# Performance work log

Hardware: AMD Instinct MI355X
Metric: run time of the kernel (lower is better)

## Reference

```python
import jax, jax.numpy as jnp
import numpy as np

SEQ, BATCH = 256, 8
N_NODES = SEQ * BATCH
VOCAB, D_MODEL, H, D_K, D_FF, N_LAYERS, MAX_POS = 259, 256, 8, 32, 1024, 2, 128


def setup_inputs() -> dict:
    key = jax.random.key(0)
    ks = jax.random.split(key, 16)
    # structured causal edge list per sequence (dst attends to src <= dst, incl. self)
    tri_dst, tri_src = np.tril_indices(SEQ)
    offs = (np.arange(BATCH) * SEQ)[:, None]
    edge_src = jnp.asarray((tri_src[None, :] + offs).ravel(), dtype=jnp.int64)
    edge_dst = jnp.asarray((tri_dst[None, :] + offs).ravel(), dtype=jnp.int64)
    positions = jnp.tile(jnp.arange(SEQ, dtype=jnp.int64), BATCH)
    tokens = jax.random.randint(ks[0], (N_NODES,), 0, VOCAB, dtype=jnp.int64)
    s = 0.02
    p = lambda k, shp: jax.random.normal(k, shp, dtype=jnp.float32) * s
    return {
        "tokens": tokens, "positions": positions,
        "edge_src": edge_src, "edge_dst": edge_dst,
        "coord_emb": p(ks[1], (3, D_MODEL)),
        "pos_emb": p(ks[2], (MAX_POS, D_MODEL)),
        "value_emb": p(ks[3], (VOCAB, D_MODEL)),
        "ln1_scale": jnp.ones((N_LAYERS, D_MODEL)), "ln1_bias": jnp.zeros((N_LAYERS, D_MODEL)),
        "Wqkv": p(ks[4], (N_LAYERS, D_MODEL, 3 * D_MODEL)),
        "Wo": p(ks[5], (N_LAYERS, D_MODEL, D_MODEL)),
        "ln2_scale": jnp.ones((N_LAYERS, D_MODEL)), "ln2_bias": jnp.zeros((N_LAYERS, D_MODEL)),
        "W1": p(ks[6], (N_LAYERS, D_MODEL, D_FF)), "b1": jnp.zeros((N_LAYERS, D_FF)),
        "W2": p(ks[7], (N_LAYERS, D_FF, D_MODEL)), "b2": jnp.zeros((N_LAYERS, D_MODEL)),
        "lnf_scale": jnp.ones((D_MODEL,)), "lnf_bias": jnp.zeros((D_MODEL,)),
        "Wg": p(ks[8], (D_MODEL, VOCAB)), "bg": jnp.zeros((VOCAB,)),
    }


def _ln(x, scale, bias, eps=1e-5):
    mu = jnp.mean(x, axis=-1, keepdims=True)
    var = jnp.var(x, axis=-1, keepdims=True)
    return (x - mu) * jax.lax.rsqrt(var + eps) * scale + bias


def _graph_attention(x, src, dst, Wqkv, Wo, ln_s, ln_b):
    n = x.shape[0]
    xn = _ln(x, ln_s, ln_b)
    qkv = (xn @ Wqkv).reshape(n, 3, H, D_K)
    q, k, v = qkv[:, 0], qkv[:, 1], qkv[:, 2]  # [n, H, D_K] each
    # u_dot_v('k','q','score') per edge, scaled
    score = jnp.einsum("ehd,ehd->eh", k[src], q[dst]) / jnp.sqrt(jnp.float32(D_K))
    # edge_softmax over incoming edges of each dst node
    smax = jax.ops.segment_max(score, dst, num_segments=n)      # [n, H]
    ex = jnp.exp(score - smax[dst])                              # [E, H]
    denom = jax.ops.segment_sum(ex, dst, num_segments=n)        # [n, H]
    alpha = ex / denom[dst]
    # u_mul_e('v','softmax_score') + sum reduce -> z on dst nodes
    z = jax.ops.segment_sum(alpha[:, :, None] * v[src], dst, num_segments=n)  # [n, H, D_K]
    return x + z.reshape(n, D_MODEL) @ Wo


def reference(tokens, positions, edge_src, edge_dst, coord_emb, pos_emb, value_emb,
              ln1_scale, ln1_bias, Wqkv, Wo, ln2_scale, ln2_bias, W1, b1, W2, b2,
              lnf_scale, lnf_bias, Wg, bg):
    x = coord_emb[positions % 3] + pos_emb[positions // 3] + value_emb[tokens]
    for i in range(Wqkv.shape[0]):
        x = _graph_attention(x, edge_src, edge_dst, Wqkv[i], Wo[i], ln1_scale[i], ln1_bias[i])
        h = _ln(x, ln2_scale[i], ln2_bias[i])
        x = x + jax.nn.relu(h @ W1[i] + b1[i]) @ W2[i] + b2[i]
    out = _ln(x, lnf_scale, lnf_bias) @ Wg + bg
    return jax.nn.log_softmax(out, axis=-1)
```

## Files before the change

### kernel.cpp

```cpp
#include <hip/hip_runtime.h>
#include <hip/hip_bf16.h>

typedef __hip_bfloat16 bf16;
typedef unsigned short ushort_t;
typedef unsigned int uint_t;
typedef __attribute__((ext_vector_type(8))) short short8;
typedef __attribute__((ext_vector_type(4))) float floatx4;

#define D_MODEL 256
#define SEQ     256
#define BATCH   8
#define NN      2048
#define NHEAD   8
#define DK      32
#define DFF     1024
#define VOCAB   259
#define NLAYER  2

#define WQKVT_OFF 0
#define WOT_OFF   393216
#define W1T_OFF   524288
#define W2T_OFF   1048576
#define WGT_OFF   1572864
#define WT_TOTAL  1639168
#define LNP_TOTAL 2560
#define BP_TOTAL  2819

__device__ __forceinline__ ushort_t f2bs(float f) {
    bf16 h = __float2bfloat16(f);
    ushort_t u; __builtin_memcpy(&u, &h, 2); return u;
}
template<bool BF>
__device__ __forceinline__ float ldw(const void* p, int i) {
    if (BF) return __bfloat162float(((const bf16*)p)[i]);
    return ((const float*)p)[i];
}
template<bool BF>
__device__ __forceinline__ ushort_t ldb(const void* p, size_t i) {
    if (BF) return ((const ushort_t*)p)[i];
    return f2bs(((const float*)p)[i]);
}
template<bool I64>
__device__ __forceinline__ int ldi(const void* p, int i) {
    if (I64) return (int)(((const long long*)p)[i]);
    return ((const int*)p)[i];
}
__device__ __forceinline__ float wred_sum(float v) {
    #pragma unroll
    for (int m = 32; m > 0; m >>= 1) v += __shfl_xor(v, m, 64);
    return v;
}
__device__ __forceinline__ float wred_max(float v) {
    #pragma unroll
    for (int m = 32; m > 0; m >>= 1) v = fmaxf(v, __shfl_xor(v, m, 64));
    return v;
}
__device__ __forceinline__ bool detBF(const void* ln1s) {
    return *(const uint_t*)ln1s == 0x3F803F80u;
}
__device__ __forceinline__ bool detI64(const void* pos) {
    const int* p32 = (const int*)pos;
    return p32[1] == 0 && p32[2] == 1;
}

template<bool BF>
__device__ void ttile(const void* src, size_t srcOff, int K, int N, int tk, int tn,
                      ushort_t* dst, ushort_t (*tile)[68]) {
    int t = threadIdx.x;
    #pragma unroll
    for (int pass = 0; pass < 16; ++pass) {
        int e = pass * 256 + t;
        int kl = e >> 6, nl = e & 63;
        int n = tn * 64 + nl;
        tile[kl][nl] = (n < N) ? ldb<BF>(src, srcOff + (size_t)(tk*64 + kl) * N + n)
                               : (ushort_t)0;
    }
    __syncthreads();
    #pragma unroll
    for (int pass = 0; pass < 16; ++pass) {
        int e = pass * 256 + t;
        int nl = e >> 6, kl = e & 63;
        int n = tn * 64 + nl;
        if (n < N) dst[(size_t)n * K + tk*64 + kl] = tile[kl][nl];
    }
}

template<bool BF, bool I64>
__device__ void embedln16(const void* tok, const void* pos,
        const void* ce, const void* pe, const void* ve,
        const void* ln1s, const void* ln1b, int rowBase,
        float* x, ushort_t* xn) {
    int lane = threadIdx.x & 63, wave = threadIdx.x >> 6;
    #pragma unroll
    for (int i = 0; i < 4; ++i) {
        int n = rowBase + wave * 4 + i;
        int p  = ldi<I64>(pos, n);
        int tk = ldi<I64>(tok, n);
        int c0 = lane * 4;
        float v[4];
        #pragma unroll
        for (int j = 0; j < 4; ++j)
            v[j] = ldw<BF>(ce, (p % 3) * 256 + c0 + j)
                 + ldw<BF>(pe, (p / 3) * 256 + c0 + j)
                 + ldw<BF>(ve, tk * 256 + c0 + j);
        float s  = wred_sum(v[0] + v[1] + v[2] + v[3]);
        float s2 = wred_sum(v[0]*v[0] + v[1]*v[1] + v[2]*v[2] + v[3]*v[3]);
        float mu = s * (1.f/256.f);
        float var = s2 * (1.f/256.f) - mu * mu;
        float rstd = rsqrtf(var + 1e-5f);
        *reinterpret_cast<float4*>(&x[(size_t)n*256 + c0]) =
            make_float4(v[0], v[1], v[2], v[3]);
        ushort4 o;
        o.x = f2bs((v[0]-mu)*rstd*ldw<BF>(ln1s, c0+0) + ldw<BF>(ln1b, c0+0));
        o.y = f2bs((v[1]-mu)*rstd*ldw<BF>(ln1s, c0+1) + ldw<BF>(ln1b, c0+1));
        o.z = f2bs((v[2]-mu)*rstd*ldw<BF>(ln1s, c0+2) + ldw<BF>(ln1b, c0+2));
        o.w = f2bs((v[3]-mu)*rstd*ldw<BF>(ln1s, c0+3) + ldw<BF>(ln1b, c0+3));
        *reinterpret_cast<ushort4*>(&xn[(size_t)n*256 + c0]) = o;
    }
}

template<bool BF, bool I64>
__device__ void prep_body(const void* tok, const void* pos,
        const void* ce, const void* pe, const void* ve,
        const void* Wqkv, const void* Wo, const void* W1, const void* W2, const void* Wg,
        const void* ln1s, const void* ln1b, const void* ln2s, const void* ln2b,
        const void* lnfs, const void* lnfb,
        const void* b1, const void* b2, const void* bg,
        ushort_t* WT, float* lnP, float* bP, float* x, ushort_t* xn,
        ushort_t (*tile)[68]) {
    int blk = blockIdx.x;
    if (blk < 404) {
        const void* src; int K, N, tk, tn; size_t dstOff, srcOff;
        if (blk < 96)       { int L = blk/48, lo = blk%48; src=Wqkv; K=256; N=768;
                              srcOff=(size_t)L*196608; dstOff=WQKVT_OFF+(size_t)L*196608;
                              tk=lo/12; tn=lo%12; }
        else if (blk < 128) { int b2=blk-96, L=b2/16, lo=b2%16; src=Wo; K=256; N=256;
                              srcOff=(size_t)L*65536; dstOff=WOT_OFF+(size_t)L*65536;
                              tk=lo/4; tn=lo%4; }
        else if (blk < 256) { int b2=blk-128, L=b2/64, lo=b2%64; src=W1; K=256; N=1024;
                              srcOff=(size_t)L*262144; dstOff=W1T_OFF+(size_t)L*262144;
                              tk=lo/16; tn=lo%16; }
        else if (blk < 384) { int b2=blk-256, L=b2/64, lo=b2%64; src=W2; K=1024; N=256;
                              srcOff=(size_t)L*262144; dstOff=W2T_OFF+(size_t)L*262144;
                              tk=lo/4; tn=lo%4; }
        else                { int lo=blk-384; src=Wg; K=256; N=259;
                              srcOff=0; dstOff=WGT_OFF; tk=lo/5; tn=lo%5; }
        ttile<BF>(src, srcOff, K, N, tk, tn, WT + dstOff, tile);
    } else if (blk < 426) {
        int gid = (blk - 404) * 256 + threadIdx.x;
        if (gid < LNP_TOTAL) {
            float v;
            if      (gid < 512)  v = ldw<BF>(ln1s, gid);
            else if (gid < 1024) v = ldw<BF>(ln1b, gid - 512);
            else if (gid < 1536) v = ldw<BF>(ln2s, gid - 1024);
            else if (gid < 2048) v = ldw<BF>(ln2b, gid - 1536);
            else if (gid < 2304) v = ldw<BF>(lnfs, gid - 2048);
            else                 v = ldw<BF>(lnfb, gid - 2304);
            lnP[gid] = v;
        } else if (gid < LNP_TOTAL + BP_TOTAL) {
            int g = gid - LNP_TOTAL;
            float v;
            if      (g < 2048) v = ldw<BF>(b1, g);
            else if (g < 2560) v = ldw<BF>(b2, g - 2048);
            else               v = ldw<BF>(bg, g - 2560);
            bP[g] = v;
        }
    } else {
        embedln16<BF, I64>(tok, pos, ce, pe, ve, ln1s, ln1b, (blk - 426) * 16, x, xn);
    }
}

__global__ void __launch_bounds__(256) prep_k(const void* tok, const void* pos,
        const void* ce, const void* pe, const void* ve,
        const void* Wqkv, const void* Wo, const void* W1, const void* W2, const void* Wg,
        const void* ln1s, const void* ln1b, const void* ln2s, const void* ln2b,
        const void* lnfs, const void* lnfb,
        const void* b1, const void* b2, const void* bg,
        ushort_t* WT, float* lnP, float* bP, float* x, ushort_t* xn) {
    __shared__ ushort_t tile[64][68];
    bool BF = detBF(ln1s), I64 = detI64(pos);
    if (BF) { if (I64) prep_body<true,true >(tok,pos,ce,pe,ve,Wqkv,Wo,W1,W2,Wg,ln1s,ln1b,ln2s,ln2b,lnfs,lnfb,b1,b2,bg,WT,lnP,bP,x,xn,tile);
              else     prep_body<true,false>(tok,pos,ce,pe,ve,Wqkv,Wo,W1,W2,Wg,ln1s,ln1b,ln2s,ln2b,lnfs,lnfb,b1,b2,bg,WT,lnP,bP,x,xn,tile); }
    else    { if (I64) prep_body<false,true >(tok,pos,ce,pe,ve,Wqkv,Wo,W1,W2,Wg,ln1s,ln1b,ln2s,ln2b,lnfs,lnfb,b1,b2,bg,WT,lnP,bP,x,xn,tile);
              else     prep_body<false,false>(tok,pos,ce,pe,ve,Wqkv,Wo,W1,W2,Wg,ln1s,ln1b,ln2s,ln2b,lnfs,lnfb,b1,b2,bg,WT,lnP,bP,x,xn,tile); }
}

union AttnSH {
    struct {
        ushort_t Ks[SEQ][40];
        ushort_t Qs[64][40];
    } a;
    ushort_t Ps[64][264];
};
__global__ void __launch_bounds__(256) attn_k(const ushort_t* __restrict__ qkvB,
                                              ushort_t* __restrict__ zB) {
    __shared__ AttnSH u;
    __shared__ ushort_t Vt[32][264];
    int t = threadIdx.x;
    int lane = t & 63, wave = t >> 6;
    int quad = lane >> 4, l16 = lane & 15;
    int tile = blockIdx.x & 3, bh = blockIdx.x >> 2;
    int b = bh >> 3, h = bh & 7;
    int base = b * SEQ;
    int dstBase = tile * 64;
    int tileEnd = (tile + 1) * 64;

    int nV = tileEnd * 4;
    for (int i = t; i < nV; i += 256) {
        int src = i >> 2, g = i & 3;
        const ushort_t* rp = qkvB + (size_t)(base + src) * 768 + h * 32 + g * 8;
        uint4 kv = *reinterpret_cast<const uint4*>(rp + 256);
        *reinterpret_cast<uint4*>(&u.a.Ks[src][g * 8]) = kv;
        uint4 vv = *reinterpret_cast<const uint4*>(rp + 512);
        const ushort_t* vs = (const ushort_t*)&vv;
        #pragma unroll
        for (int j = 0; j < 8; ++j) Vt[g * 8 + j][src] = vs[j];
    }
    {
        int r = t >> 2, g = t & 3;
        uint4 qv = *reinterpret_cast<const uint4*>(
            qkvB + (size_t)(base + dstBase + r) * 768 + h * 32 + g * 8);
        *reinterpret_cast<uint4*>(&u.a.Qs[r][g * 8]) = qv;
    }
    __syncthreads();

    const float scale = 0.17677669529663687f;
    int stLim = tile * 4 + wave;
    int stCnt = stLim + 1;
    short8 qf = *reinterpret_cast<const short8*>(&u.a.Qs[wave * 16 + l16][quad * 8]);
    floatx4 accs[16];
    #pragma unroll
    for (int st = 0; st < 16; ++st) {
        if (st <= stLim) {
            short8 kf = *reinterpret_cast<const short8*>(&u.a.Ks[st * 16 + l16][quad * 8]);
            accs[st] = __builtin_amdgcn_mfma_f32_16x16x32_bf16(qf, kf, (floatx4){0.f,0.f,0.f,0.f}, 0, 0, 0);
        }
    }
    float mrow[4] = {-3e38f, -3e38f, -3e38f, -3e38f};
    #pragma unroll
    for (int st = 0; st < 16; ++st) {
        if (st <= stLim) {
            int srcg = st * 16 + l16;
            #pragma unroll
            for (int r = 0; r < 4; ++r) {
                int dstg = dstBase + wave * 16 + quad * 4 + r;
                float sv = (srcg <= dstg) ? accs[st][r] * scale : -3e38f;
                accs[st][r] = sv;
                mrow[r] = fmaxf(mrow[r], sv);
            }
        }
    }
    #pragma unroll
    for (int mk = 1; mk < 16; mk <<= 1)
        #pragma unroll
        for (int r = 0; r < 4; ++r) mrow[r] = fmaxf(mrow[r], __shfl_xor(mrow[r], mk, 64));
    float lrow[4] = {0.f, 0.f, 0.f, 0.f};
    #pragma unroll
    for (int st = 0; st < 16; ++st) {
        if (st <= stLim) {
            #pragma unroll
            for (int r = 0; r < 4; ++r) {
                float p = __expf(accs[st][r] - mrow[r]);
                accs[st][r] = p;
                lrow[r] += p;
            }
        }
    }
    #pragma unroll
    for (int mk = 1; mk < 16; mk <<= 1)
        #pragma unroll
        for (int r = 0; r < 4; ++r) lrow[r] += __shfl_xor(lrow[r], mk, 64);
    __syncthreads();

    #pragma unroll
    for (int st = 0; st < 16; ++st) {
        if (st <= stLim) {
            #pragma unroll
            for (int r = 0; r < 4; ++r)
                u.Ps[wave * 16 + quad * 4 + r][st * 16 + l16] = f2bs(accs[st][r]);
        }
    }
    if (stCnt & 1) {
        #pragma unroll
        for (int r = 0; r < 4; ++r)
            u.Ps[wave * 16 + quad * 4 + r][stCnt * 16 + l16] = 0;
    }
    __syncthreads();

    int ktCnt = (stCnt + 1) >> 1;
    floatx4 acco[2];
    acco[0] = (floatx4){0.f,0.f,0.f,0.f};
    acco[1] = (floatx4){0.f,0.f,0.f,0.f};
    #pragma unroll
    for (int kt = 0; kt < 8; ++kt) {
        if (kt < ktCnt) {
            short8 pf = *reinterpret_cast<const short8*>(&u.Ps[wave * 16 + l16][kt * 32 + quad * 8]);
            #pragma unroll
            for (int dn = 0; dn < 2; ++dn) {
                short8 vf = *reinterpret_cast<const short8*>(&Vt[dn * 16 + l16][kt * 32 + quad * 8]);
                acco[dn] = __builtin_amdgcn_mfma_f32_16x16x32_bf16(pf, vf, acco[dn], 0, 0, 0);
            }
        }
    }
    #pragma unroll
    for (int dn = 0; dn < 2; ++dn)
        #pragma unroll
        for (int r = 0; r < 4; ++r)
            zB[(size_t)(base + dstBase + wave * 16 + quad * 4 + r) * 256
               + h * 32 + dn * 16 + l16] = f2bs(acco[dn][r] / lrow[r]);
}

__global__ void __launch_bounds__(256) gemm_k(const ushort_t* __restrict__ A, int K,
        const ushort_t* __restrict__ BT, const float* __restrict__ bias,
        ushort_t* __restrict__ C, int ldc, int relu) {
    int t = threadIdx.x;
    int lane = t & 63, wave = t >> 6;
    int quad = lane >> 4, l16 = lane & 15;
    int wm = (wave >> 1) * 32, wn = (wave & 1) * 32;
    int rowBase = blockIdx.x * 64, colBase = blockIdx.y * 64;
    floatx4 acc[2][2];
    #pragma unroll
    for (int a = 0; a < 2; ++a)
        #pragma unroll
        for (int b = 0; b < 2; ++b) acc[a][b] = (floatx4){0.f,0.f,0.f,0.f};
    const ushort_t* a0 = A + (size_t)(rowBase + wm + l16) * K + quad * 8;
    const ushort_t* a1 = a0 + (size_t)16 * K;
    const ushort_t* b0 = BT + (size_t)(colBase + wn + l16) * K + quad * 8;
    const ushort_t* b1 = b0 + (size_t)16 * K;
    #pragma unroll 8
    for (int k0 = 0; k0 < K; k0 += 32) {
        short8 af0 = *reinterpret_cast<const short8*>(a0 + k0);
        short8 af1 = *reinterpret_cast<const short8*>(a1 + k0);
        short8 bf0 = *reinterpret_cast<const short8*>(b0 + k0);
        short8 bf1 = *reinterpret_cast<const short8*>(b1 + k0);
        acc[0][0] = __builtin_amdgcn_mfma_f32_16x16x32_bf16(af0, bf0, acc[0][0], 0,0,0);
        acc[0][1] = __builtin_amdgcn_mfma_f32_16x16x32_bf16(af0, bf1, acc[0][1], 0,0,0);
        acc[1][0] = __builtin_amdgcn_mfma_f32_16x16x32_bf16(af1, bf0, acc[1][0], 0,0,0);
        acc[1][1] = __builtin_amdgcn_mfma_f32_16x16x32_bf16(af1, bf1, acc[1][1], 0,0,0);
    }
    #pragma unroll
    for (int nt = 0; nt < 2; ++nt) {
        int col = colBase + wn + nt*16 + l16;
        float bb = bias ? bias[col] : 0.f;
        #pragma unroll
        for (int mt = 0; mt < 2; ++mt)
            #pragma unroll
            for (int r = 0; r < 4; ++r) {
                int row = rowBase + wm + mt*16 + quad*4 + r;
                float v = acc[mt][nt][r] + bb;
                if (relu) v = fmaxf(v, 0.f);
                C[(size_t)row * ldc + col] = f2bs(v);
            }
    }
}

__global__ void __launch_bounds__(256) woff1_k(
        const ushort_t* __restrict__ zB, const ushort_t* __restrict__ WoT,
        const float* __restrict__ xIn, float* __restrict__ xOut,
        const float* __restrict__ ls2, const float* __restrict__ lb2,
        const ushort_t* __restrict__ W1T, const float* __restrict__ b1P,
        ushort_t* __restrict__ hmidG) {
    __shared__ float    xrow[32][256];
    __shared__ ushort_t xnA[32][264];
    int t = threadIdx.x, lane = t & 63, wave = t >> 6;
    int quad = lane >> 4, l16 = lane & 15;
    int rowBase = blockIdx.x * 32, cg = blockIdx.y;

    {
        floatx4 acc[2][4];
        #pragma unroll
        for (int mt = 0; mt < 2; ++mt)
            #pragma unroll
            for (int nt = 0; nt < 4; ++nt) acc[mt][nt] = (floatx4){0.f,0.f,0.f,0.f};
        const ushort_t* a0 = zB + (size_t)(rowBase + l16) * 256 + quad * 8;
        const ushort_t* a1 = a0 + (size_t)16 * 256;
        #pragma unroll
        for (int k0 = 0; k0 < 256; k0 += 32) {
            short8 af0 = *reinterpret_cast<const short8*>(a0 + k0);
            short8 af1 = *reinterpret_cast<const short8*>(a1 + k0);
            #pragma unroll
            for (int nt = 0; nt < 4; ++nt) {
                short8 bv = *reinterpret_cast<const short8*>(
                    WoT + (size_t)(wave*64 + nt*16 + l16) * 256 + k0 + quad * 8);
                acc[0][nt] = __builtin_amdgcn_mfma_f32_16x16x32_bf16(af0, bv, acc[0][nt], 0,0,0);
                acc[1][nt] = __builtin_amdgcn_mfma_f32_16x16x32_bf16(af1, bv, acc[1][nt], 0,0,0);
            }
        }
        #pragma unroll
        for (int nt = 0; nt < 4; ++nt) {
            int col = wave*64 + nt*16 + l16;
            #pragma unroll
            for (int mt = 0; mt < 2; ++mt)
                #pragma unroll
                for (int r = 0; r < 4; ++r) {
                    int row = mt*16 + quad*4 + r;
                    float v = acc[mt][nt][r] + xIn[(size_t)(rowBase + row) * 256 + col];
                    xOut[(size_t)(rowBase + row) * 256 + col] = v;
                    xrow[row][col] = v;
                }
        }
    }
    __syncthreads();
    #pragma unroll
    for (int i = 0; i < 8; ++i) {
        int row = wave*8 + i, c0 = lane * 4;
        float4 vv = *reinterpret_cast<const float4*>(&xrow[row][c0]);
        float s  = wred_sum(vv.x + vv.y + vv.z + vv.w);
        float s2 = wred_sum(vv.x*vv.x + vv.y*vv.y + vv.z*vv.z + vv.w*vv.w);
        float mu = s * (1.f/256.f);
        float var = s2 * (1.f/256.f) - mu*mu;
        float rstd = rsqrtf(var + 1e-5f);
        ushort4 o;
        o.x = f2bs((vv.x-mu)*rstd*ls2[c0+0] + lb2[c0+0]);
        o.y = f2bs((vv.y-mu)*rstd*ls2[c0+1] + lb2[c0+1]);
        o.z = f2bs((vv.z-mu)*rstd*ls2[c0+2] + lb2[c0+2]);
        o.w = f2bs((vv.w-mu)*rstd*ls2[c0+3] + lb2[c0+3]);
        *reinterpret_cast<ushort4*>(&xnA[row][c0]) = o;
    }
    __syncthreads();
    {
        floatx4 acc[2][4];
        #pragma unroll
        for (int mt = 0; mt < 2; ++mt)
            #pragma unroll
            for (int nt = 0; nt < 4; ++nt) acc[mt][nt] = (floatx4){0.f,0.f,0.f,0.f};
        const ushort_t* a0 = &xnA[l16][quad * 8];
        const ushort_t* a1 = &xnA[16 + l16][quad * 8];
        #pragma unroll
        for (int k0 = 0; k0 < 256; k0 += 32) {
            short8 af0 = *reinterpret_cast<const short8*>(a0 + k0);
            short8 af1 = *reinterpret_cast<const short8*>(a1 + k0);
            #pragma unroll
            for (int nt = 0; nt < 4; ++nt) {
                short8 bv = *reinterpret_cast<const short8*>(
                    W1T + (size_t)(cg*256 + wave*64 + nt*16 + l16) * 256 + k0 + quad * 8);
                acc[0][nt] = __builtin_amdgcn_mfma_f32_16x16x32_bf16(af0, bv, acc[0][nt], 0,0,0);
                acc[1][nt] = __builtin_amdgcn_mfma_f32_16x16x32_bf16(af1, bv, acc[1][nt], 0,0,0);
            }
        }
        #pragma unroll
        for (int nt = 0; nt < 4; ++nt) {
            int col = cg*256 + wave*64 + nt*16 + l16;
            float bb = b1P[col];
            #pragma unroll
            for (int mt = 0; mt < 2; ++mt)
                #pragma unroll
                for (int r = 0; r < 4; ++r) {
                    int row = mt*16 + quad*4 + r;
                    hmidG[(size_t)(rowBase + row) * 1024 + col] =
                        f2bs(fmaxf(acc[mt][nt][r] + bb, 0.f));
                }
        }
    }
}

__global__ void __launch_bounds__(256) w2_k(
        const ushort_t* __restrict__ hmidG, const ushort_t* __restrict__ W2T,
        const float* __restrict__ b2P,
        const float* __restrict__ xPre, float* __restrict__ yOut) {
    int t = threadIdx.x, lane = t & 63, wave = t >> 6;
    int quad = lane >> 4, l16 = lane & 15;
    int rowBase = blockIdx.x * 32, colBase = blockIdx.y * 64;
    int wm = (wave >> 1) * 16, wn = (wave & 1) * 32;
    floatx4 acc[2];
    acc[0] = (floatx4){0.f,0.f,0.f,0.f};
    acc[1] = (floatx4){0.f,0.f,0.f,0.f};
    const ushort_t* a0 = hmidG + (size_t)(rowBase + wm + l16) * 1024 + quad * 8;
    #pragma unroll 8
    for (int k0 = 0; k0 < 1024; k0 += 32) {
        short8 af = *reinterpret_cast<const short8*>(a0 + k0);
        #pragma unroll
        for (int nt = 0; nt < 2; ++nt) {
            short8 bv = *reinterpret_cast<const short8*>(
                W2T + (size_t)(colBase + wn + nt*16 + l16) * 1024 + k0 + quad * 8);
            acc[nt] = __builtin_amdgcn_mfma_f32_16x16x32_bf16(af, bv, acc[nt], 0,0,0);
        }
    }
    #pragma unroll
    for (int nt = 0; nt < 2; ++nt) {
        int col = colBase + wn + nt*16 + l16;
        float bb = b2P[col];
        #pragma unroll
        for (int r = 0; r < 4; ++r) {
            int row = wm + quad*4 + r;
            float v = acc[nt][r] + bb + xPre[(size_t)(rowBase + row) * 256 + col];
            yOut[(size_t)(rowBase + row) * 256 + col] = v;
        }
    }
}

__global__ void __launch_bounds__(256) lnqkv_k(
        const float* __restrict__ yIn,
        const float* __restrict__ ls, const float* __restrict__ lb,
        const ushort_t* __restrict__ WqkvT, ushort_t* __restrict__ qkvB) {
    __shared__ ushort_t xnA[64][264];
    int t = threadIdx.x, lane = t & 63, wave = t >> 6;
    int quad = lane >> 4, l16 = lane & 15;
    int rowBase = blockIdx.x * 64, colBase = blockIdx.y * 64;
    #pragma unroll
    for (int i = 0; i < 16; ++i) {
        int row = wave*16 + i, c0 = lane * 4;
        float4 vv = *reinterpret_cast<const float4*>(yIn + (size_t)(rowBase + row) * 256 + c0);
        float s  = wred_sum(vv.x + vv.y + vv.z + vv.w);
        float s2 = wred_sum(vv.x*vv.x + vv.y*vv.y + vv.z*vv.z + vv.w*vv.w);
        float mu = s * (1.f/256.f);
        float var = s2 * (1.f/256.f) - mu*mu;
        float rstd = rsqrtf(var + 1e-5f);
        ushort4 o;
        o.x = f2bs((vv.x-mu)*rstd*ls[c0+0] + lb[c0+0]);
        o.y = f2bs((vv.y-mu)*rstd*ls[c0+1] + lb[c0+1]);
        o.z = f2bs((vv.z-mu)*rstd*ls[c0+2] + lb[c0+2]);
        o.w = f2bs((vv.w-mu)*rstd*ls[c0+3] + lb[c0+3]);
        *reinterpret_cast<ushort4*>(&xnA[row][c0]) = o;
    }
    __syncthreads();
    int wm = (wave >> 1) * 32, wn = (wave & 1) * 32;
    floatx4 acc[2][2];
    #pragma unroll
    for (int a = 0; a < 2; ++a)
        #pragma unroll
        for (int b = 0; b < 2; ++b) acc[a][b] = (floatx4){0.f,0.f,0.f,0.f};
    const ushort_t* a0 = &xnA[wm + l16][quad * 8];
    const ushort_t* a1 = &xnA[wm + 16 + l16][quad * 8];
    #pragma unroll
    for (int k0 = 0; k0 < 256; k0 += 32) {
        short8 af0 = *reinterpret_cast<const short8*>(a0 + k0);
        short8 af1 = *reinterpret_cast<const short8*>(a1 + k0);
        #pragma unroll
        for (int nt = 0; nt < 2; ++nt) {
            short8 bv = *reinterpret_cast<const short8*>(
                WqkvT + (size_t)(colBase + wn + nt*16 + l16) * 256 + k0 + quad * 8);
            acc[0][nt] = __builtin_amdgcn_mfma_f32_16x16x32_bf16(af0, bv, acc[0][nt], 0,0,0);
            acc[1][nt] = __builtin_amdgcn_mfma_f32_16x16x32_bf16(af1, bv, acc[1][nt], 0,0,0);
        }
    }
    #pragma unroll
    for (int nt = 0; nt < 2; ++nt) {
        int col = colBase + wn + nt*16 + l16;
        #pragma unroll
        for (int mt = 0; mt < 2; ++mt)
            #pragma unroll
            for (int r = 0; r < 4; ++r) {
                int row = wm + mt*16 + quad*4 + r;
                qkvB[(size_t)(rowBase + row) * 768 + col] = f2bs(acc[mt][nt][r]);
            }
    }
}

__global__ void __launch_bounds__(256) lnlg_k(
        const float* __restrict__ yIn,
        const float* __restrict__ lnfsP, const float* __restrict__ lnfbP,
        const ushort_t* __restrict__ WgT, const float* __restrict__ bgP,
        const void* __restrict__ ln1sRaw, void* __restrict__ outp) {
    __shared__ float    xrow[16][256];
    __shared__ ushort_t xnA[16][264];
    __shared__ float    Lg[16][273];
    int t = threadIdx.x, lane = t & 63, wave = t >> 6;
    int quad = lane >> 4, l16 = lane & 15;
    int rowBase = blockIdx.x * 16;
    #pragma unroll
    for (int i = 0; i < 4; ++i) {
        int idx = i * 256 + t;
        int row = idx >> 6, c4 = (idx & 63) * 4;
        *reinterpret_cast<float4*>(&xrow[row][c4]) =
            *reinterpret_cast<const float4*>(yIn + (size_t)(rowBase + row) * 256 + c4);
    }
    __syncthreads();
    #pragma unroll
    for (int i = 0; i < 4; ++i) {
        int row = wave*4 + i, c0 = lane * 4;
        float4 vv = *reinterpret_cast<const float4*>(&xrow[row][c0]);
        float s  = wred_sum(vv.x + vv.y + vv.z + vv.w);
        float s2 = wred_sum(vv.x*vv.x + vv.y*vv.y + vv.z*vv.z + vv.w*vv.w);
        float mu = s * (1.f/256.f);
        float var = s2 * (1.f/256.f) - mu*mu;
        float rstd = rsqrtf(var + 1e-5f);
        ushort4 o;
        o.x = f2bs((vv.x-mu)*rstd*lnfsP[c0+0] + lnfbP[c0+0]);
        o.y = f2bs((vv.y-mu)*rstd*lnfsP[c0+1] + lnfbP[c0+1]);
        o.z = f2bs((vv.z-mu)*rstd*lnfsP[c0+2] + lnfbP[c0+2]);
        o.w = f2bs((vv.w-mu)*rstd*lnfsP[c0+3] + lnfbP[c0+3]);
        *reinterpret_cast<ushort4*>(&xnA[row][c0]) = o;
    }
    __syncthreads();
    const ushort_t* a0 = &xnA[l16][quad * 8];
    int cb = wave * 64;
    {
        floatx4 acc[4];
        #pragma unroll
        for (int nt = 0; nt < 4; ++nt) acc[nt] = (floatx4){0.f,0.f,0.f,0.f};
        #pragma unroll
        for (int kc = 0; kc < 8; ++kc) {
            short8 af = *reinterpret_cast<const short8*>(a0 + kc * 32);
            #pragma unroll
            for (int nt = 0; nt < 4; ++nt) {
                short8 bv = *reinterpret_cast<const short8*>(
                    WgT + (size_t)(cb + nt*16 + l16) * 256 + kc*32 + quad*8);
                acc[nt] = __builtin_amdgcn_mfma_f32_16x16x32_bf16(af, bv, acc[nt], 0,0,0);
            }
        }
        #pragma unroll
        for (int nt = 0; nt < 4; ++nt) {
            int col = cb + nt*16 + l16;
            float bb = bgP[col];
            #pragma unroll
            for (int r = 0; r < 4; ++r)
                Lg[quad*4 + r][col] = acc[nt][r] + bb;
        }
    }
    if (wave == 0) {
        floatx4 acc = (floatx4){0.f,0.f,0.f,0.f};
        int n = 256 + l16;
        int nc = (n < VOCAB) ? n : 0;
        const ushort_t* b0 = WgT + (size_t)nc * 256 + quad * 8;
        #pragma unroll
        for (int kc = 0; kc < 8; ++kc) {
            short8 af = *reinterpret_cast<const short8*>(a0 + kc * 32);
            short8 bv = *reinterpret_cast<const short8*>(b0 + kc * 32);
            acc = __builtin_amdgcn_mfma_f32_16x16x32_bf16(af, bv, acc, 0,0,0);
        }
        #pragma unroll
        for (int r = 0; r < 4; ++r)
            Lg[quad*4 + r][256 + l16] = (n < VOCAB) ? (acc[r] + bgP[n]) : -1e30f;
    }
    __syncthreads();
    int outBF = detBF(ln1sRaw) ? 1 : 0;
    #pragma unroll
    for (int i = 0; i < 4; ++i) {
        int row = wave*4 + i;
        float v0 = Lg[row][lane],     v1 = Lg[row][lane+64];
        float v2 = Lg[row][lane+128], v3 = Lg[row][lane+192];
        float v4 = (lane < 16) ? Lg[row][256+lane] : -1e30f;
        float m = wred_max(fmaxf(fmaxf(fmaxf(v0,v1), fmaxf(v2,v3)), v4));
        float se = __expf(v0-m) + __expf(v1-m) + __expf(v2-m) + __expf(v3-m)
                 + ((lane < 16) ? __expf(v4-m) : 0.f);
        se = wred_sum(se);
        float lse = m + logf(se);
        size_t nbase = (size_t)(rowBase + row) * VOCAB;
        if (outBF) {
            ushort_t* o = (ushort_t*)outp + nbase;
            o[lane]     = f2bs(v0 - lse);
            o[lane+64]  = f2bs(v1 - lse);
            o[lane+128] = f2bs(v2 - lse);
            o[lane+192] = f2bs(v3 - lse);
            if (lane < 3) o[256+lane] = f2bs(v4 - lse);
        } else {
            float* o = (float*)outp + nbase;
            o[lane]     = v0 - lse;
            o[lane+64]  = v1 - lse;
            o[lane+128] = v2 - lse;
            o[lane+192] = v3 - lse;
            if (lane < 3) o[256+lane] = v4 - lse;
        }
    }
}

extern "C" void kernel_launch(void* const* d_in, const int* in_sizes, int n_in,
                              void* d_out, int out_size, void* d_ws, size_t ws_size,
                              hipStream_t stream) {
    const void* tok  = d_in[0];
    const void* pos  = d_in[1];
    const void* ce   = d_in[4];
    const void* pe   = d_in[5];
    const void* ve   = d_in[6];
    const void* ln1s = d_in[7];
    const void* ln1b = d_in[8];
    const void* Wqkv = d_in[9];
    const void* Wo   = d_in[10];
    const void* ln2s = d_in[11];
    const void* ln2b = d_in[12];
    const void* W1   = d_in[13];
    const void* b1   = d_in[14];
    const void* W2   = d_in[15];
    const void* b2   = d_in[16];
    const void* lnfs = d_in[17];
    const void* lnfb = d_in[18];
    const void* Wg   = d_in[19];
    const void* bg   = d_in[20];

    char* base = (char*)d_ws;
    float*    lnP   = (float*)base;
    float*    bP    = (float*)(base + 10240);
    float*    xA    = (float*)(base + 22528);
    ushort_t* xn    = (ushort_t*)(base + 2119680);
    ushort_t* zB    = (ushort_t*)(base + 3168256);
    ushort_t* hmidG = (ushort_t*)(base + 4216832);
    ushort_t* WT    = (ushort_t*)(base + 8411136);
    ushort_t* qkvB  = (ushort_t*)(base + 11689472);
    float*    xB    = (float*)(base + 14835200);
    float*    xC    = (float*)(base + 16932352);

    prep_k<<<554, 256, 0, stream>>>(tok, pos, ce, pe, ve,
        Wqkv, Wo, W1, W2, Wg, ln1s, ln1b, ln2s, ln2b, lnfs, lnfb,
        b1, b2, bg, WT, lnP, bP, xA, xn);

    gemm_k<<<dim3(32, 12), 256, 0, stream>>>(xn, 256,
        WT + WQKVT_OFF, nullptr, qkvB, 768, 0);

    attn_k<<<256, 256, 0, stream>>>(qkvB, zB);

    woff1_k<<<dim3(64, 4), 256, 0, stream>>>(zB, WT + WOT_OFF, xA, xB,
        lnP + 1024, lnP + 1536, WT + W1T_OFF, bP, hmidG);
    w2_k<<<dim3(64, 4), 256, 0, stream>>>(hmidG, WT + W2T_OFF, bP + 2048, xB, xC);

    lnqkv_k<<<dim3(32, 12), 256, 0, stream>>>(xC, lnP + 256, lnP + 768,
        WT + WQKVT_OFF + 196608, qkvB);

    attn_k<<<256, 256, 0, stream>>>(qkvB, zB);

    woff1_k<<<dim3(64, 4), 256, 0, stream>>>(zB, WT + WOT_OFF + 65536, xC, xA,
        lnP + 1024 + 256, lnP + 1536 + 256, WT + W1T_OFF + 262144, bP + 1024, hmidG);
    w2_k<<<dim3(64, 4), 256, 0, stream>>>(hmidG, WT + W2T_OFF + 262144,
        bP + 2048 + 256, xA, xB);

    lnlg_k<<<128, 256, 0, stream>>>(xB, lnP + 2048, lnP + 2304,
        WT + WGT_OFF, bP + 2560, ln1s, d_out);
}
```

Before: 212.0 us.

## Fuse FFN down-projection into Wo/W1 kernel with split-K atomic accumulation

Merges the W2 GEMM into the Wo+LN2+W1 kernel: each column-group block keeps its 256-wide slice of the hidden activation in shared memory and computes a split-K partial of W2, accumulated into the output with float atomics. The attention kernel zeroes the output buffer beforehand, and the cg==0 block adds the residual and bias. This removes one launch per layer and the global round-trip of the hidden activation. It also vectorizes the weight-transpose prep path for 64-aligned widths. The atomics add contention and make the summation order nondeterministic.

Measured after the change: 204.3 us. 1.04x faster.

```diff
diff --git a/kernel.cpp b/kernel.cpp
--- a/kernel.cpp
+++ b/kernel.cpp
@@ -65,23 +65,55 @@
 
 template<bool BF>
 __device__ void ttile(const void* src, size_t srcOff, int K, int N, int tk, int tn,
-                      ushort_t* dst, ushort_t (*tile)[68]) {
+                      ushort_t* dst, ushort_t (*tile)[72]) {
     int t = threadIdx.x;
-    #pragma unroll
-    for (int pass = 0; pass < 16; ++pass) {
-        int e = pass * 256 + t;
-        int kl = e >> 6, nl = e & 63;
-        int n = tn * 64 + nl;
-        tile[kl][nl] = (n < N) ? ldb<BF>(src, srcOff + (size_t)(tk*64 + kl) * N + n)
-                               : (ushort_t)0;
-    }
-    __syncthreads();
-    #pragma unroll
-    for (int pass = 0; pass < 16; ++pass) {
-        int e = pass * 256 + t;
-        int nl = e >> 6, kl = e & 63;
-        int n = tn * 64 + nl;
-        if (n < N) dst[(size_t)n * K + tk*64 + kl] = tile[kl][nl];
+    if ((N & 63) == 0) {
+        #pragma unroll
+        for (int pass = 0; pass < 2; ++pass) {
+            int e = pass * 256 + t;
+            int kl = e >> 3, ng = e & 7;
+            size_t sbase = srcOff + (size_t)(tk*64 + kl) * N + tn*64 + ng*8;
+            ushort_t v[8];
+            if (BF) {
+                *reinterpret_cast<uint4*>(v) =
+                    *reinterpret_cast<const uint4*>((const ushort_t*)src + sbase);
+            } else {
+                float4 a = *reinterpret_cast<const float4*>((const float*)src + sbase);
+                float4 b = *reinterpret_cast<const float4*>((const float*)src + sbase + 4);
+                v[0]=f2bs(a.x); v[1]=f2bs(a.y); v[2]=f2bs(a.z); v[3]=f2bs(a.w);
+                v[4]=f2bs(b.x); v[5]=f2bs(b.y); v[6]=f2bs(b.z); v[7]=f2bs(b.w);
+            }
+            *reinterpret_cast<uint4*>(&tile[kl][ng*8]) = *reinterpret_cast<const uint4*>(v);
+        }
+        __syncthreads();
+        #pragma unroll
+        for (int pass = 0; pass < 2; ++pass) {
+            int e = pass * 256 + t;
+            int nl = e >> 3, kg = e & 7;
+            int n = tn * 64 + nl;
+            ushort_t v[8];
+            #pragma unroll
+            for (int j = 0; j < 8; ++j) v[j] = tile[kg*8 + j][nl];
+            *reinterpret_cast<uint4*>(dst + (size_t)n * K + tk*64 + kg*8) =
+                *reinterpret_cast<const uint4*>(v);
+        }
+    } else {
+        #pragma unroll
+        for (int pass = 0; pass < 16; ++pass) {
+            int e = pass * 256 + t;
+            int kl = e >> 6, nl = e & 63;
+            int n = tn * 64 + nl;
+            tile[kl][nl] = (n < N) ? ldb<BF>(src, srcOff + (size_t)(tk*64 + kl) * N + n)
+                                   : (ushort_t)0;
+        }
+        __syncthreads();
+        #pragma unroll
+        for (int pass = 0; pass < 16; ++pass) {
+            int e = pass * 256 + t;
+            int nl = e >> 6, kl = e & 63;
+            int n = tn * 64 + nl;
+            if (n < N) dst[(size_t)n * K + tk*64 + kl] = tile[kl][nl];
+        }
     }
 }
 
@@ -127,7 +159,7 @@
         const void* lnfs, const void* lnfb,
         const void* b1, const void* b2, const void* bg,
         ushort_t* WT, float* lnP, float* bP, float* x, ushort_t* xn,
-        ushort_t (*tile)[68]) {
+        ushort_t (*tile)[72]) {
     int blk = blockIdx.x;
     if (blk < 404) {
         const void* src; int K, N, tk, tn; size_t dstOff, srcOff;
@@ -177,7 +209,7 @@
         const void* lnfs, const void* lnfb,
         const void* b1, const void* b2, const void* bg,
         ushort_t* WT, float* lnP, float* bP, float* x, ushort_t* xn) {
-    __shared__ ushort_t tile[64][68];
+    __shared__ ushort_t tile[64][72];
     bool BF = detBF(ln1s), I64 = detI64(pos);
     if (BF) { if (I64) prep_body<true,true >(tok,pos,ce,pe,ve,Wqkv,Wo,W1,W2,Wg,ln1s,ln1b,ln2s,ln2b,lnfs,lnfb,b1,b2,bg,WT,lnP,bP,x,xn,tile);
               else     prep_body<true,false>(tok,pos,ce,pe,ve,Wqkv,Wo,W1,W2,Wg,ln1s,ln1b,ln2s,ln2b,lnfs,lnfb,b1,b2,bg,WT,lnP,bP,x,xn,tile); }
@@ -193,10 +225,17 @@
     ushort_t Ps[64][264];
 };
 __global__ void __launch_bounds__(256) attn_k(const ushort_t* __restrict__ qkvB,
-                                              ushort_t* __restrict__ zB) {
+                                              ushort_t* __restrict__ zB,
+                                              float* __restrict__ yZ) {
     __shared__ AttnSH u;
     __shared__ ushort_t Vt[32][264];
     int t = threadIdx.x;
+    {
+        float4 z4 = make_float4(0.f, 0.f, 0.f, 0.f);
+        float4* yp = reinterpret_cast<float4*>(yZ + (size_t)blockIdx.x * 2048);
+        yp[t]       = z4;
+        yp[t + 256] = z4;
+    }
     int lane = t & 63, wave = t >> 6;
     int quad = lane >> 4, l16 = lane & 15;
     int tile = blockIdx.x & 3, bh = blockIdx.x >> 2;
@@ -354,17 +393,20 @@
     }
 }
 
-__global__ void __launch_bounds__(256) woff1_k(
+__global__ void __launch_bounds__(256) tail_k(
         const ushort_t* __restrict__ zB, const ushort_t* __restrict__ WoT,
-        const float* __restrict__ xIn, float* __restrict__ xOut,
+        const float* __restrict__ xIn,
         const float* __restrict__ ls2, const float* __restrict__ lb2,
         const ushort_t* __restrict__ W1T, const float* __restrict__ b1P,
-        ushort_t* __restrict__ hmidG) {
-    __shared__ float    xrow[32][256];
+        const ushort_t* __restrict__ W2T, const float* __restrict__ b2P,
+        float* __restrict__ yAcc) {
+    __shared__ float    xrowS[32][256];
     __shared__ ushort_t xnA[32][264];
+    ushort_t (*hmidS)[264] = reinterpret_cast<ushort_t (*)[264]>(&xrowS[0][0]);
     int t = threadIdx.x, lane = t & 63, wave = t >> 6;
     int quad = lane >> 4, l16 = lane & 15;
     int rowBase = blockIdx.x * 32, cg = blockIdx.y;
+    float vpre[2][4][4];
 
     {
         floatx4 acc[2][4];
@@ -395,8 +437,8 @@
                 for (int r = 0; r < 4; ++r) {
                     int row = mt*16 + quad*4 + r;
                     float v = acc[mt][nt][r] + xIn[(size_t)(rowBase + row) * 256 + col];
-                    xOut[(size_t)(rowBase + row) * 256 + col] = v;
-                    xrow[row][col] = v;
+                    vpre[mt][nt][r] = v;
+                    xrowS[row][col] = v;
                 }
         }
     }
@@ -404,7 +446,7 @@
     #pragma unroll
     for (int i = 0; i < 8; ++i) {
         int row = wave*8 + i, c0 = lane * 4;
-        float4 vv = *reinterpret_cast<const float4*>(&xrow[row][c0]);
+        float4 vv = *reinterpret_cast<const float4*>(&xrowS[row][c0]);
         float s  = wred_sum(vv.x + vv.y + vv.z + vv.w);
         float s2 = wred_sum(vv.x*vv.x + vv.y*vv.y + vv.z*vv.z + vv.w*vv.w);
         float mu = s * (1.f/256.f);
@@ -418,6 +460,7 @@
         *reinterpret_cast<ushort4*>(&xnA[row][c0]) = o;
     }
     __syncthreads();
+
     {
         floatx4 acc[2][4];
         #pragma unroll
@@ -438,53 +481,55 @@
                 acc[1][nt] = __builtin_amdgcn_mfma_f32_16x16x32_bf16(af1, bv, acc[1][nt], 0,0,0);
             }
         }
+        __syncthreads();
         #pragma unroll
         for (int nt = 0; nt < 4; ++nt) {
-            int col = cg*256 + wave*64 + nt*16 + l16;
-            float bb = b1P[col];
+            int lcol = wave*64 + nt*16 + l16;
+            float bb = b1P[cg*256 + lcol];
             #pragma unroll
             for (int mt = 0; mt < 2; ++mt)
                 #pragma unroll
                 for (int r = 0; r < 4; ++r) {
                     int row = mt*16 + quad*4 + r;
-                    hmidG[(size_t)(rowBase + row) * 1024 + col] =
-                        f2bs(fmaxf(acc[mt][nt][r] + bb, 0.f));
+                    hmidS[row][lcol] = f2bs(fmaxf(acc[mt][nt][r] + bb, 0.f));
                 }
         }
     }
-}
-
-__global__ void __launch_bounds__(256) w2_k(
-        const ushort_t* __restrict__ hmidG, const ushort_t* __restrict__ W2T,
-        const float* __restrict__ b2P,
-        const float* __restrict__ xPre, float* __restrict__ yOut) {
-    int t = threadIdx.x, lane = t & 63, wave = t >> 6;
-    int quad = lane >> 4, l16 = lane & 15;
-    int rowBase = blockIdx.x * 32, colBase = blockIdx.y * 64;
-    int wm = (wave >> 1) * 16, wn = (wave & 1) * 32;
-    floatx4 acc[2];
-    acc[0] = (floatx4){0.f,0.f,0.f,0.f};
-    acc[1] = (floatx4){0.f,0.f,0.f,0.f};
-    const ushort_t* a0 = hmidG + (size_t)(rowBase + wm + l16) * 1024 + quad * 8;
-    #pragma unroll 8
-    for (int k0 = 0; k0 < 1024; k0 += 32) {
-        short8 af = *reinterpret_cast<const short8*>(a0 + k0);
-        #pragma unroll
-        for (int nt = 0; nt < 2; ++nt) {
-            short8 bv = *reinterpret_cast<const short8*>(
-                W2T + (size_t)(colBase + wn + nt*16 + l16) * 1024 + k0 + quad * 8);
-            acc[nt] = __builtin_amdgcn_mfma_f32_16x16x32_bf16(af, bv, acc[nt], 0,0,0);
-        }
-    }
-    #pragma unroll
-    for (int nt = 0; nt < 2; ++nt) {
-        int col = colBase + wn + nt*16 + l16;
-        float bb = b2P[col];
-        #pragma unroll
-        for (int r = 0; r < 4; ++r) {
-            int row = wm + quad*4 + r;
-            float v = acc[nt][r] + bb + xPre[(size_t)(rowBase + row) * 256 + col];
-            yOut[(size_t)(rowBase + row) * 256 + col] = v;
+    __syncthreads();
+
+    {
+        floatx4 acc[2][4];
+        #pragma unroll
+        for (int mt = 0; mt < 2; ++mt)
+            #pragma unroll
+            for (int nt = 0; nt < 4; ++nt) acc[mt][nt] = (floatx4){0.f,0.f,0.f,0.f};
+        const ushort_t* a0 = &hmidS[l16][quad * 8];
+        const ushort_t* a1 = &hmidS[16 + l16][quad * 8];
+        #pragma unroll
+        for (int k0 = 0; k0 < 256; k0 += 32) {
+            short8 af0 = *reinterpret_cast<const short8*>(a0 + k0);
+            short8 af1 = *reinterpret_cast<const short8*>(a1 + k0);
+            #pragma unroll
+            for (int nt = 0; nt < 4; ++nt) {
+                short8 bv = *reinterpret_cast<const short8*>(
+                    W2T + (size_t)(wave*64 + nt*16 + l16) * 1024 + cg*256 + k0 + quad * 8);
+                acc[0][nt] = __builtin_amdgcn_mfma_f32_16x16x32_bf16(af0, bv, acc[0][nt], 0,0,0);
+                acc[1][nt] = __builtin_amdgcn_mfma_f32_16x16x32_bf16(af1, bv, acc[1][nt], 0,0,0);
+            }
+        }
+        #pragma unroll
+        for (int nt = 0; nt < 4; ++nt) {
+            int col = wave*64 + nt*16 + l16;
+            float bb = (cg == 0) ? b2P[col] : 0.f;
+            #pragma unroll
+            for (int mt = 0; mt < 2; ++mt)
+                #pragma unroll
+                for (int r = 0; r < 4; ++r) {
+                    int row = mt*16 + quad*4 + r;
+                    float add = acc[mt][nt][r];
+                    if (cg == 0) add += vpre[mt][nt][r] + bb;
+                    atomicAdd(&yAcc[(size_t)(rowBase + row) * 256 + col], add);
+                }
         }
     }
 }
@@ -684,7 +729,6 @@
     float*    xA    = (float*)(base + 22528);
     ushort_t* xn    = (ushort_t*)(base + 2119680);
     ushort_t* zB    = (ushort_t*)(base + 3168256);
-    ushort_t* hmidG = (ushort_t*)(base + 4216832);
     ushort_t* WT    = (ushort_t*)(base + 8411136);
     ushort_t* qkvB  = (ushort_t*)(base + 11689472);
     float*    xB    = (float*)(base + 14835200);
@@ -697,22 +741,20 @@
     gemm_k<<<dim3(32, 12), 256, 0, stream>>>(xn, 256,
         WT + WQKVT_OFF, nullptr, qkvB, 768, 0);
 
-    attn_k<<<256, 256, 0, stream>>>(qkvB, zB);
-
-    woff1_k<<<dim3(64, 4), 256, 0, stream>>>(zB, WT + WOT_OFF, xA, xB,
-        lnP + 1024, lnP + 1536, WT + W1T_OFF, bP, hmidG);
-    w2_k<<<dim3(64, 4), 256, 0, stream>>>(hmidG, WT + W2T_OFF, bP + 2048, xB, xC);
-
-    lnqkv_k<<<dim3(32, 12), 256, 0, stream>>>(xC, lnP + 256, lnP + 768,
+    attn_k<<<256, 256, 0, stream>>>(qkvB, zB, xB);
+
+    tail_k<<<dim3(64, 4), 256, 0, stream>>>(zB, WT + WOT_OFF, xA,
+        lnP + 1024, lnP + 1536, WT + W1T_OFF, bP, WT + W2T_OFF, bP + 2048, xB);
+
+    lnqkv_k<<<dim3(32, 12), 256, 0, stream>>>(xB, lnP + 256, lnP + 768,
         WT + WQKVT_OFF + 196608, qkvB);
 
-    attn_k<<<256, 256, 0, stream>>>(qkvB, zB);
-
-    woff1_k<<<dim3(64, 4), 256, 0, stream>>>(zB, WT + WOT_OFF + 65536, xC, xA,
-        lnP + 1024 + 256, lnP + 1536 + 256, WT + W1T_OFF + 262144, bP + 1024, hmidG);
-    w2_k<<<dim3(64, 4), 256, 0, stream>>>(hmidG, WT + W2T_OFF + 262144,
-        bP + 2048 + 256, xA, xB);
-
-    lnlg_k<<<128, 256, 0, stream>>>(xB, lnP + 2048, lnP + 2304,
+    attn_k<<<256, 256, 0, stream>>>(qkvB, zB, xC);
+
+    tail_k<<<dim3(64, 4), 256, 0, stream>>>(zB, WT + WOT_OFF + 65536, xB,
+        lnP + 1024 + 256, lnP + 1536 + 256, WT + W1T_OFF + 262144, bP + 1024,
+        WT + W2T_OFF + 262144, bP + 2048 + 256, xC);
+
+    lnlg_k<<<128, 256, 0, stream>>>(xC, lnP + 2048, lnP + 2304,
         WT + WGT_OFF, bP + 2560, ln1s, d_out);
 }
```
